# Optimization experiments

Measured on AMD Instinct MI355X. Metric: run time of the kernel, lower is better.

## Reference

```python
import jax, jax.numpy as jnp
import numpy as np

B, N, D, H, T, DFF, OUT = 32, 256, 512, 8, 60, 2048, 2
EPS = 1e-5


def _mha(q, k, v, Wq, Wk, Wv, Wo, bq, bk, bv, bo):
    # torch nn.MultiheadAttention (batch_first): x @ W.T + b projections
    Bq, Lq, Dm = q.shape
    dh = Dm // H
    scale = 1.0 / np.sqrt(dh).astype(np.float32)
    qh = (q @ Wq.T + bq).reshape(Bq, Lq, H, dh).transpose(0, 2, 1, 3)
    kh = (k @ Wk.T + bk).reshape(Bq, k.shape[1], H, dh).transpose(0, 2, 1, 3)
    vh = (v @ Wv.T + bv).reshape(Bq, v.shape[1], H, dh).transpose(0, 2, 1, 3)
    a = jax.nn.softmax(jnp.einsum('bhqd,bhkd->bhqk', qh, kh) * scale, axis=-1)
    o = jnp.einsum('bhqk,bhkd->bhqd', a, vh).transpose(0, 2, 1, 3).reshape(Bq, Lq, Dm)
    return o @ Wo.T + bo


def _ln(x, w, b):
    m = x.mean(-1, keepdims=True)
    v = ((x - m) ** 2).mean(-1, keepdims=True)
    return (x - m) / jnp.sqrt(v + EPS) * w + b


def setup_inputs() -> dict:
    key = jax.random.key(0)
    ks = iter(jax.random.split(key, 64))

    def rn(shape, s=0.05):
        return jax.random.normal(next(ks), shape, dtype=jnp.float32) * s

    inp = {
        'H_v_all': rn((B, N, D), 1.0),
        'H_v0_init': rn((B, 1, 1, D), 1.0),
        'pe': rn((1, T, D), 1.0),  # positional_encoding parameter
    }
    # s_* : spatial_attn;  sa_* : decoder self-attn;  ca_* : decoder cross-attn
    for p in ('s', 'sa', 'ca'):
        for m in ('Wq', 'Wk', 'Wv', 'Wo'):
            inp[f'{p}_{m}'] = rn((D, D))
        for m in ('bq', 'bk', 'bv', 'bo'):
            inp[f'{p}_{m}'] = jnp.zeros((D,), jnp.float32)
    for i in (1, 2, 3):
        inp[f'ln{i}_w'] = jnp.ones((D,), jnp.float32)
        inp[f'ln{i}_b'] = jnp.zeros((D,), jnp.float32)
    inp['W1'] = rn((DFF, D)); inp['b1'] = jnp.zeros((DFF,), jnp.float32)
    inp['W2'] = rn((D, DFF)); inp['b2'] = jnp.zeros((D,), jnp.float32)
    inp['Wout'] = rn((OUT, D)); inp['bout'] = jnp.zeros((OUT,), jnp.float32)
    return inp


def reference(H_v_all, H_v0_init, pe,
              s_Wq, s_Wk, s_Wv, s_Wo, s_bq, s_bk, s_bv, s_bo,
              sa_Wq, sa_Wk, sa_Wv, sa_Wo, sa_bq, sa_bk, sa_bv, sa_bo,
              ca_Wq, ca_Wk, ca_Wv, ca_Wo, ca_bq, ca_bk, ca_bv, ca_bo,
              ln1_w, ln1_b, ln2_w, ln2_b, ln3_w, ln3_b,
              W1, b1, W2, b2, Wout, bout):

    def dec_layer(x, mem):
        # post-norm TransformerDecoderLayer, no masks (non-causal), relu FFN, eval (no dropout)
        sa = _mha(x, x, x, sa_Wq, sa_Wk, sa_Wv, sa_Wo, sa_bq, sa_bk, sa_bv, sa_bo)
        x = _ln(x + sa, ln1_w, ln1_b)
        ca = _mha(x, mem, mem, ca_Wq, ca_Wk, ca_Wv, ca_Wo, ca_bq, ca_bk, ca_bv, ca_bo)
        x = _ln(x + ca, ln2_w, ln2_b)
        ff = jax.nn.relu(x @ W1.T + b1) @ W2.T + b2
        return _ln(x + ff, ln3_w, ln3_b)

    tgt = H_v0_init  # (B, 1, 1, D), grows along dim 2
    outputs = []
    for t in range(T):
        tgt_pe = tgt + pe[:, :t + 1][:, None]        # (B,1,t+1,D)
        tgt_step = tgt_pe.reshape(B, t + 1, D)
        ctx = _mha(tgt_step[:, -1:, :], H_v_all, H_v_all,
                   s_Wq, s_Wk, s_Wv, s_Wo, s_bq, s_bk, s_bv, s_bo)
        decoded = dec_layer(tgt_step, H_v_all)
        nxt = decoded[:, -1:, :] + ctx               # (B,1,D)
        tgt = jnp.concatenate([tgt, nxt[:, None]], axis=2)
        outputs.append(nxt[:, None])                 # (B,1,1,D)
    out_seq = jnp.concatenate(outputs, axis=2)       # (B,1,T,D)
    return out_seq @ Wout.T + bout                   # (B,1,T,2)
```

## Files before the change

kernel.cpp:

```cpp
#include <hip/hip_runtime.h>


#define NB 32
#define NN 256
#define DD 512
#define NH 8
#define DH 64
#define TT 60
#define DF 2048
#define NBLK 256
#define NTHR 512

typedef unsigned short ushort_t;
typedef _Float16 half2v __attribute__((ext_vector_type(2)));

constexpr size_t SZ_KV  = (size_t)NB * NN * DD;
constexpr size_t SZ_ROW = (size_t)NB * DD;
constexpr size_t SZ_PAR = (size_t)NB * NH * DD;
constexpr size_t OFF_KS32 = 0;
constexpr size_t OFF_VS32 = SZ_KV;
constexpr size_t OFF_KC32 = 2 * SZ_KV;
constexpr size_t OFF_VC32 = 3 * SZ_KV;
constexpr size_t OFF_X    = 0;
constexpr size_t OFF_U1P  = OFF_X   + SZ_ROW;
constexpr size_t OFF_U2P  = OFF_U1P + SZ_PAR;
constexpr size_t OFF_U3P  = OFF_U2P + SZ_PAR;
constexpr size_t OFF_CTP0 = OFF_U3P + SZ_PAR;
constexpr size_t OFF_CTP1 = OFF_CTP0 + SZ_PAR;
constexpr size_t OFF_BF   = 4 * SZ_KV;
constexpr size_t UOFF_KST = 0;
constexpr size_t UOFF_KCT = SZ_KV;
constexpr size_t UOFF_VSH = 2 * SZ_KV;
constexpr size_t UOFF_VCH = 3 * SZ_KV;
constexpr size_t UOFF_W8  = 4 * SZ_KV;
constexpr size_t UOFF_W1  = UOFF_W8 + 8ull * DD * DD;
constexpr size_t UOFF_W2  = UOFF_W1 + (size_t)DD * DF;
constexpr size_t UEND     = UOFF_W2 + (size_t)DF * DD;
constexpr size_t OFF_FLG  = OFF_BF + (UEND + 1) / 2;

constexpr unsigned DYN_LDS = 131072;

__device__ __forceinline__ float ldg_a(const float* p) {
  return __hip_atomic_load(p, __ATOMIC_RELAXED, __HIP_MEMORY_SCOPE_AGENT);
}
__device__ __forceinline__ void stg_a(float* p, float v) {
  __hip_atomic_store(p, v, __ATOMIC_RELAXED, __HIP_MEMORY_SCOPE_AGENT);
}
__device__ __forceinline__ unsigned f2pk(float a, float b) {
  return __builtin_bit_cast(unsigned, __builtin_amdgcn_cvt_pkrtz(a, b));
}
__device__ __forceinline__ ushort_t f2h(float a) {
  return (ushort_t)(f2pk(a, 0.f) & 0xffffu);
}
__device__ __forceinline__ float h2f(ushort_t u) {
  return (float)__builtin_bit_cast(_Float16, u);
}
__device__ __forceinline__ float fdot2u(unsigned a, unsigned b, float c) {
  return __builtin_amdgcn_fdot2(__builtin_bit_cast(half2v, a),
                                __builtin_bit_cast(half2v, b), c, false);
}

struct Params {
  const float *pe;
  const float *sa_bq, *sa_bk, *sa_bv, *s_bq, *sa_bo, *s_bo, *ca_bq, *ca_bo;
  const float *ln1w, *ln1b, *ln2w, *ln2b, *ln3w, *ln3b;
  const float *b1, *b2, *Wout, *bout;
  const ushort_t *w8, *w1b, *w2b;
  const ushort_t *KsT, *KcT, *VsH, *VcH;
  float *xcur, *u1p, *u2p, *u3p, *ctp0, *ctp1;
  float *out;
  unsigned *flags;
};

__device__ __forceinline__ void set_flag(unsigned* fl, int tid, int h,
                                         unsigned val) {
  __builtin_amdgcn_s_waitcnt(0);
  __syncthreads();
  if (tid == 0)
    __hip_atomic_store(&fl[h], val, __ATOMIC_RELAXED,
                       __HIP_MEMORY_SCOPE_AGENT);
}
__device__ __forceinline__ void wait_ge(unsigned* fl, int tid,
                                        unsigned target) {
  if (tid < 64) {
    bool wait = true;
    while (wait) {
      unsigned v = target;
      if (tid < 8)
        v = __hip_atomic_load(&fl[tid], __ATOMIC_RELAXED,
                              __HIP_MEMORY_SCOPE_AGENT);
      wait = __any(v < target);
    }
  }
  __syncthreads();
}

__global__ __launch_bounds__(512) void decode_persistent(Params P) {
  __shared__ __align__(16) float sX[2048];
  __shared__ __align__(16) float sPart[512];
  __shared__ float sAux[64];
  __shared__ __align__(16) unsigned xh[256];
  __shared__ __align__(16) unsigned ph[384];
  __shared__ __align__(16) ushort_t cacheK[TT * 78];
  __shared__ __align__(16) ushort_t cacheV[TT * 64];
  extern __shared__ __align__(16) unsigned dynLds[];
  unsigned* Ks_l = dynLds;
  unsigned* Kc_l = dynLds + 8192;
  ushort_t* Vs_l = (ushort_t*)(dynLds + 16384);
  ushort_t* Vc_l = Vs_l + 16384;

  int tid = threadIdx.x;
  int bid = blockIdx.x;
  int b = bid >> 3, h = bid & 7;
  int idx8 = bid;
  unsigned* fl = P.flags + b * 64;
  unsigned rnd = 0;

  {
    const uint4* gks = (const uint4*)((const unsigned*)P.KsT +
                       (((size_t)b * DD + h * DH) >> 1) * NN);
    const uint4* gkc = (const uint4*)((const unsigned*)P.KcT +
                       (((size_t)b * DD + h * DH) >> 1) * NN);
    const uint4* gvs = (const uint4*)(P.VsH + (size_t)idx8 * NN * DH);
    const uint4* gvc = (const uint4*)(P.VcH + (size_t)idx8 * NN * DH);
    uint4* dks = (uint4*)Ks_l;
    uint4* dkc = (uint4*)Kc_l;
    uint4* dvs = (uint4*)Vs_l;
    uint4* dvc = (uint4*)Vc_l;
    #pragma unroll
    for (int i = 0; i < 4; i++) {
      int idx = i * NTHR + tid;
      dks[idx] = gks[idx];
      dkc[idx] = gkc[idx];
      dvs[idx] = gvs[idx];
      dvc[idx] = gvc[idx];
    }
  }

  float x_f = ldg_a(P.xcur + (size_t)b * DD + tid);
  {
    float px = __shfl_xor(x_f, 1);
    if (!(tid & 1)) xh[tid >> 1] = f2pk(x_f, px);
  }
  __syncthreads();

  for (int t = 0; t < TT; t++) {
    {
      {
        int w = tid >> 6, c = tid & 63, m = w >> 1, half = w & 1;
        int col = h * DH + c;
        const uint2* wp = (const uint2*)(P.w8 + (size_t)m * DD * DD) + col;
        float acc = 0.f;
        #pragma unroll 8
        for (int kq = half * 64; kq < half * 64 + 64; kq++) {
          uint2 wv = wp[(size_t)kq * DD];
          uint2 xv = *(const uint2*)&xh[kq * 2];
          acc = fdot2u(wv.x, xv.x, acc);
          acc = fdot2u(wv.y, xv.y, acc);
        }
        sPart[tid] = acc;
      }
      __syncthreads();
      if (tid < 256) {
        int m = tid >> 6, c = tid & 63, col = h * DH + c;
        const float* bias = (m == 0) ? P.sa_bq : (m == 1) ? P.sa_bk
                          : (m == 2) ? P.sa_bv : P.s_bq;
        float val = sPart[(2 * m) * 64 + c] + sPart[(2 * m + 1) * 64 + c]
                    + bias[col];
        sX[512 + tid] = val;
        if (m == 1) cacheK[t * 78 + c] = f2h(val);
        if (m == 2) cacheV[t * 64 + c] = f2h(val);
      }
      __syncthreads();

      int L = t + 1;
      float* sQ  = sX + 512;
      float* sQs = sX + 704;
      float* sPb = sX + 768;
      if (tid < 64) {
        float e = 0.f;
        if (tid < L) {
          const unsigned* kl = (const unsigned*)(cacheK + (size_t)tid * 78);
          float a = 0.f;
          #pragma unroll 8
          for (int i = 0; i < 32; i++) {
            unsigned w = kl[i];
            a += sQ[2 * i] * h2f((ushort_t)(w & 0xffffu)) +
                 sQ[2 * i + 1] * h2f((ushort_t)(w >> 16));
          }
          e = __expf(a * 0.125f);
        }
        float s2 = e;
        #pragma unroll
        for (int s = 32; s >= 1; s >>= 1) s2 += __shfl_xor(s2, s);
        sPb[tid] = e * (1.f / s2);
        float o = 0.f;
        for (int j = 0; j < L; j++)
          o += sPb[j] * h2f(cacheV[j * 64 + tid]);
        float po = __shfl_xor(o, 1);
        if (!(tid & 1)) ph[32 + (tid >> 1)] = f2pk(o, po);
      } else if (tid < 320) {
        int n = tid - 64;
        float a = 0.f;
        #pragma unroll 8
        for (int i = 0; i < 32; i++) {
          unsigned w = Ks_l[i * NN + n];
          a += sQs[2 * i] * h2f((ushort_t)(w & 0xffffu)) +
               sQs[2 * i + 1] * h2f((ushort_t)(w >> 16));
        }
        sPart[n] = a * 0.125f;
      }
      __syncthreads();
      {
        float* u1p = P.u1p + ((size_t)b * NH + h) * DD;
        const uint2* wpa = (const uint2*)(P.w8 + 4ull * DD * DD) + tid;
        float acc1 = (h == 0) ? P.sa_bo[tid] + x_f : 0.f;
        #pragma unroll 8
        for (int j = 0; j < 16; j++) {
          int k4 = h * 16 + j;
          uint2 wv = wpa[(size_t)k4 * DD];
          uint2 x1 = *(const uint2*)&ph[32 + 2 * j];
          acc1 = fdot2u(wv.x, x1.x, acc1);
          acc1 = fdot2u(wv.y, x1.y, acc1);
        }
        stg_a(&u1p[tid], acc1);
      }
      set_flag(fl, tid, h, 3 * t + 1);
      float* sPr = sX + 1536;
      if (tid < 256) {
        float e = __expf(sPart[tid]);
        sPr[tid] = e;
        int w = tid >> 6;
        float s2 = e;
        #pragma unroll
        for (int s = 32; s >= 1; s >>= 1) s2 += __shfl_xor(s2, s);
        if ((tid & 63) == 0) sAux[4 + w] = s2;
      }
      __syncthreads();
      float* sB = sX + 1024;
      {
        int g = tid >> 6, d = tid & 63;
        float inv = 1.f / (sAux[4] + sAux[5] + sAux[6] + sAux[7]);
        const ushort_t* vp = Vs_l + (g * 32) * DH + d;
        float acc = 0.f;
        #pragma unroll 4
        for (int n = 0; n < 32; n++) acc += sPr[g * 32 + n] * h2f(vp[n * DH]);
        sB[tid] = acc * inv;
      }
      __syncthreads();
      if (tid < 64) {
        float o = 0.f;
        #pragma unroll
        for (int i = 0; i < 8; i++) o += sB[i * 64 + tid];
        float po = __shfl_xor(o, 1);
        if (!(tid & 1)) ph[64 + (tid >> 1)] = f2pk(o, po);
      }
      __syncthreads();
      {
        float* ctp = ((t & 1) ? P.ctp1 : P.ctp0) + ((size_t)b * NH + h) * DD;
        const uint2* wpb = (const uint2*)(P.w8 + 5ull * DD * DD) + tid;
        float acc2 = (h == 0) ? P.s_bo[tid] : 0.f;
        #pragma unroll 8
        for (int j = 0; j < 16; j++) {
          int k4 = h * 16 + j;
          uint2 wv2 = wpb[(size_t)k4 * DD];
          uint2 x2 = *(const uint2*)&ph[64 + 2 * j];
          acc2 = fdot2u(wv2.x, x2.x, acc2);
          acc2 = fdot2u(wv2.y, x2.y, acc2);
        }
        stg_a(&ctp[tid], acc2);
      }
    }

    float y1f;
    {
      wait_ge(fl, tid, 3 * t + 1);
      float u = 0.f;
      {
        const float* pp = P.u1p + (size_t)b * NH * DD + tid;
        #pragma unroll
        for (int i = 0; i < 8; i++) u += ldg_a(pp + i * DD);
      }
      {
        int w = tid >> 6;
        float s = u, q2 = u * u;
        #pragma unroll
        for (int m = 32; m >= 1; m >>= 1) { s += __shfl_xor(s, m); q2 += __shfl_xor(q2, m); }
        if ((tid & 63) == 0) { sAux[w] = s; sAux[8 + w] = q2; }
      }
      __syncthreads();
      {
        float ss = 0.f, qq = 0.f;
        #pragma unroll
        for (int i = 0; i < 8; i++) { ss += sAux[i]; qq += sAux[8 + i]; }
        float mean = ss * (1.f / 512.f);
        float inv = rsqrtf(qq * (1.f / 512.f) - mean * mean + 1e-5f);
        y1f = (u - mean) * inv * P.ln1w[tid] + P.ln1b[tid];
        float py = __shfl_xor(y1f, 1);
        if (!(tid & 1)) ph[128 + (tid >> 1)] = f2pk(y1f, py);
      }
      __syncthreads();
      {
        int c = tid & 63, w = tid >> 6, col = h * DH + c;
        const uint2* wp = (const uint2*)(P.w8 + 6ull * DD * DD) + col;
        float acc = 0.f;
        #pragma unroll 8
        for (int kq = w * 16; kq < w * 16 + 16; kq++) {
          uint2 wv = wp[(size_t)kq * DD];
          uint2 xv = *(const uint2*)&ph[128 + 2 * kq];
          acc = fdot2u(wv.x, xv.x, acc);
          acc = fdot2u(wv.y, xv.y, acc);
        }
        sPart[tid] = acc;
      }
      __syncthreads();
      if (tid < 64) {
        float o = 0.f;
        #pragma unroll
        for (int i = 0; i < 8; i++) o += sPart[i * 64 + tid];
        o += P.ca_bq[h * DH + tid];
        float po = __shfl_xor(o, 1);
        if (!(tid & 1)) ph[tid >> 1] = f2pk(o, po);
      }
      __syncthreads();
      {
        int n = tid & 255, dh2 = tid >> 8;
        float a = 0.f;
        #pragma unroll 8
        for (int dw = dh2 * 16; dw < dh2 * 16 + 16; dw++)
          a = fdot2u(Kc_l[dw * NN + n], ph[dw], a);
        sPart[tid] = a;
      }
      __syncthreads();
      float* sPr = sX + 1536;
      if (tid < 256) {
        float e = __expf((sPart[tid] + sPart[256 + tid]) * 0.125f);
        sPr[tid] = e;
        int w = tid >> 6;
        float s2 = e;
        #pragma unroll
        for (int s = 32; s >= 1; s >>= 1) s2 += __shfl_xor(s2, s);
        if ((tid & 63) == 0) sAux[4 + w] = s2;
      }
      __syncthreads();
      float* sB = sX + 1024;
      {
        int g = tid >> 6, d = tid & 63;
        float inv = 1.f / (sAux[4] + sAux[5] + sAux[6] + sAux[7]);
        const ushort_t* vp = Vc_l + (g * 32) * DH + d;
        float acc = 0.f;
        #pragma unroll 4
        for (int n = 0; n < 32; n++) acc += sPr[g * 32 + n] * h2f(vp[n * DH]);
        sB[tid] = acc * inv;
      }
      __syncthreads();
      if (tid < 64) {
        float o = 0.f;
        #pragma unroll
        for (int i = 0; i < 8; i++) o += sB[i * 64 + tid];
        float po = __shfl_xor(o, 1);
        if (!(tid & 1)) ph[32 + (tid >> 1)] = f2pk(o, po);
      }
      __syncthreads();
      {
        const uint2* wp = (const uint2*)(P.w8 + 7ull * DD * DD) + tid;
        float acc = (h == 0) ? P.ca_bo[tid] + y1f : 0.f;
        #pragma unroll 8
        for (int j = 0; j < 16; j++) {
          int k4 = h * 16 + j;
          uint2 wv = wp[(size_t)k4 * DD];
          uint2 xv = *(const uint2*)&ph[32 + 2 * j];
          acc = fdot2u(wv.x, xv.x, acc);
          acc = fdot2u(wv.y, xv.y, acc);
        }
        stg_a(&P.u2p[((size_t)b * NH + h) * DD + tid], acc);
      }
    }
    set_flag(fl, tid, h, 3 * t + 2);

    float zf;
    {
      wait_ge(fl, tid, 3 * t + 2);
      float v = 0.f;
      {
        const float* pp = P.u2p + (size_t)b * NH * DD + tid;
        #pragma unroll
        for (int i = 0; i < 8; i++) v += ldg_a(pp + i * DD);
      }
      {
        int w = tid >> 6;
        float s = v, q2 = v * v;
        #pragma unroll
        for (int m = 32; m >= 1; m >>= 1) { s += __shfl_xor(s, m); q2 += __shfl_xor(q2, m); }
        if ((tid & 63) == 0) { sAux[w] = s; sAux[8 + w] = q2; }
      }
      __syncthreads();
      {
        float ss = 0.f, qq = 0.f;
        #pragma unroll
        for (int i = 0; i < 8; i++) { ss += sAux[i]; qq += sAux[8 + i]; }
        float mean = ss * (1.f / 512.f);
        float inv = rsqrtf(qq * (1.f / 512.f) - mean * mean + 1e-5f);
        zf = (v - mean) * inv * P.ln2w[tid] + P.ln2b[tid];
        float pz = __shfl_xor(zf, 1);
        if (!(tid & 1)) ph[128 + (tid >> 1)] = f2pk(zf, pz);
      }
      __syncthreads();
      {
        int c = tid & 255, half = tid >> 8, col = h * 256 + c;
        const uint2* wp = (const uint2*)P.w1b + col;
        float acc = 0.f;
        #pragma unroll 8
        for (int kq = half * 64; kq < half * 64 + 64; kq++) {
          uint2 wv = wp[(size_t)kq * DF];
          uint2 xv = *(const uint2*)&ph[128 + 2 * kq];
          acc = fdot2u(wv.x, xv.x, acc);
          acc = fdot2u(wv.y, xv.y, acc);
        }
        sPart[tid] = acc;
      }
      __syncthreads();
      if (tid < 256) {
        float hv = fmaxf(sPart[tid] + sPart[256 + tid] + P.b1[h * 256 + tid], 0.f);
        float pv = __shfl_xor(hv, 1);
        if (!(tid & 1)) ph[tid >> 1] = f2pk(hv, pv);
      }
      __syncthreads();
      {
        const uint2* wp = (const uint2*)P.w2b + tid;
        float acc = (h == 0) ? zf + P.b2[tid] : 0.f;
        #pragma unroll 8
        for (int j = 0; j < 64; j++) {
          int k4 = h * 64 + j;
          uint2 wv = wp[(size_t)k4 * DD];
          uint2 xv = *(const uint2*)&ph[2 * j];
          acc = fdot2u(wv.x, xv.x, acc);
          acc = fdot2u(wv.y, xv.y, acc);
        }
        stg_a(&P.u3p[((size_t)b * NH + h) * DD + tid], acc);
      }
    }
    set_flag(fl, tid, h, 3 * t + 3);

    {
      wait_ge(fl, tid, 3 * t + 3);
      float u = 0.f, ctxv = 0.f;
      {
        const float* pp = P.u3p + (size_t)b * NH * DD + tid;
        const float* cp = ((t & 1) ? P.ctp1 : P.ctp0) + (size_t)b * NH * DD + tid;
        #pragma unroll
        for (int i = 0; i < 8; i++) { u += ldg_a(pp + i * DD); ctxv += ldg_a(cp + i * DD); }
      }
      {
        int w = tid >> 6;
        float s = u, q2 = u * u;
        #pragma unroll
        for (int m = 32; m >= 1; m >>= 1) { s += __shfl_xor(s, m); q2 += __shfl_xor(q2, m); }
        if ((tid & 63) == 0) { sAux[w] = s; sAux[8 + w] = q2; }
      }
      __syncthreads();
      float ss = 0.f, qq = 0.f;
      #pragma unroll
      for (int i = 0; i < 8; i++) { ss += sAux[i]; qq += sAux[8 + i]; }
      float mean = ss * (1.f / 512.f);
      float inv = rsqrtf(qq * (1.f / 512.f) - mean * mean + 1e-5f);
      float nxt = (u - mean) * inv * P.ln3w[tid] + P.ln3b[tid] + ctxv;
      float p = (t < TT - 1) ? P.pe[(size_t)(t + 1) * DD + tid] : 0.f;
      x_f = nxt + p;
      {
        float px = __shfl_xor(x_f, 1);
        if (!(tid & 1)) xh[tid >> 1] = f2pk(x_f, px);
      }
      if (h == 0) sX[tid] = nxt;
      __syncthreads();
      if (h == 0) {
        {
          int c = tid >> 8, l = tid & 255;
          float a = sX[l] * P.Wout[(size_t)c * DD + l] +
                    sX[l + 256] * P.Wout[(size_t)c * DD + l + 256];
          #pragma unroll
          for (int m = 32; m >= 1; m >>= 1) a += __shfl_xor(a, m);
          if ((tid & 63) == 0) sAux[16 + (tid >> 6)] = a;
        }
        __syncthreads();
        if (tid == 0)
          P.out[((size_t)b * TT + t) * 2 + 0] =
              sAux[16] + sAux[17] + sAux[18] + sAux[19] + P.bout[0];
        if (tid == 256)
          P.out[((size_t)b * TT + t) * 2 + 1] =
              sAux[20] + sAux[21] + sAux[22] + sAux[23] + P.bout[1];
      }
      __syncthreads();
    }
  }
  (void)rnd;
}

__global__ __launch_bounds__(256) void gemm_kv(
    const float* __restrict__ A,
    const float* __restrict__ W0, const float* __restrict__ W1_,
    const float* __restrict__ W2_, const float* __restrict__ W3_,
    const float* __restrict__ b0, const float* __restrict__ b1_,
    const float* __restrict__ b2_, const float* __restrict__ b3_,
    float* __restrict__ O0, float* __restrict__ O1,
    float* __restrict__ O2, float* __restrict__ O3) {
  __shared__ __align__(16) float As[8][128];
  __shared__ __align__(16) float Bs[8][128];
  int tid = threadIdx.x;
  int bx = blockIdx.x, by = blockIdx.y;
  int mm = bx >> 2;
  int col0 = (bx & 3) * 128;
  const float* W = mm == 0 ? W0 : mm == 1 ? W1_ : mm == 2 ? W2_ : W3_;
  const float* bias = mm == 0 ? b0 : mm == 1 ? b1_ : mm == 2 ? b2_ : b3_;
  float* O = mm == 0 ? O0 : mm == 1 ? O1 : mm == 2 ? O2 : O3;
  int tx = tid & 15, ty = tid >> 4;
  int m0 = by * 128;
  int lr = tid >> 1, lk = (tid & 1) * 4;
  const float* Ap = A + (size_t)(m0 + lr) * DD + lk;
  const float* Wp = W + (size_t)(col0 + lr) * DD + lk;
  float c[8][8] = {};
  for (int k0 = 0; k0 < DD; k0 += 8) {
    float4 av = *(const float4*)(Ap + k0);
    float4 wv = *(const float4*)(Wp + k0);
    __syncthreads();
    As[lk + 0][lr] = av.x; As[lk + 1][lr] = av.y; As[lk + 2][lr] = av.z; As[lk + 3][lr] = av.w;
    Bs[lk + 0][lr] = wv.x; Bs[lk + 1][lr] = wv.y; Bs[lk + 2][lr] = wv.z; Bs[lk + 3][lr] = wv.w;
    __syncthreads();
    #pragma unroll
    for (int k = 0; k < 8; k++) {
      float a[8], bb[8];
      *(float4*)&a[0] = *(const float4*)&As[k][ty * 8];
      *(float4*)&a[4] = *(const float4*)&As[k][ty * 8 + 4];
      *(float4*)&bb[0] = *(const float4*)&Bs[k][tx * 8];
      *(float4*)&bb[4] = *(const float4*)&Bs[k][tx * 8 + 4];
      #pragma unroll
      for (int i = 0; i < 8; i++)
        #pragma unroll
        for (int j = 0; j < 8; j++) c[i][j] += a[i] * bb[j];
    }
  }
  const float* bp = bias + col0 + tx * 8;
  for (int i = 0; i < 8; i++) {
    int row = m0 + ty * 8 + i;
    float* op = O + (size_t)row * DD + col0 + tx * 8;
    #pragma unroll
    for (int jq = 0; jq < 8; jq += 4) {
      float4 v;
      v.x = c[i][jq + 0] + bp[jq + 0];
      v.y = c[i][jq + 1] + bp[jq + 1];
      v.z = c[i][jq + 2] + bp[jq + 2];
      v.w = c[i][jq + 3] + bp[jq + 3];
      *(float4*)(op + jq) = v;
    }
  }
}

__global__ __launch_bounds__(256) void pack_kT(const float* __restrict__ Ks32,
                                               const float* __restrict__ Kc32,
                                               ushort_t* __restrict__ KsT,
                                               ushort_t* __restrict__ KcT) {
  int z = blockIdx.z;
  int b = z >> 1;
  const float* in = ((z & 1) ? Kc32 : Ks32) + (size_t)b * NN * DD;
  ushort_t* out = ((z & 1) ? KcT : KsT) + (size_t)b * NN * DD;
  int r0 = blockIdx.x * 32, c0 = blockIdx.y * 32;
  __shared__ float tile[32][33];
  int tid = threadIdx.x;
  int i = tid >> 3, j4 = (tid & 7) * 4;
  float4 v = *(const float4*)(in + (size_t)(r0 + i) * DD + c0 + j4);
  tile[i][j4] = v.x; tile[i][j4 + 1] = v.y; tile[i][j4 + 2] = v.z; tile[i][j4 + 3] = v.w;
  __syncthreads();
  int d = c0 + i;
  ushort_t* op = out + (size_t)(d >> 1) * (2 * NN) + 2 * (r0 + j4) + (d & 1);
  op[0] = f2h(tile[j4][i]);     op[2] = f2h(tile[j4 + 1][i]);
  op[4] = f2h(tile[j4 + 2][i]); op[6] = f2h(tile[j4 + 3][i]);
}

__global__ __launch_bounds__(256) void pack_vh(const float* __restrict__ Vs32,
                                               const float* __restrict__ Vc32,
                                               ushort_t* __restrict__ VsH,
                                               ushort_t* __restrict__ VcH) {
  const float* src = blockIdx.y ? Vc32 : Vs32;
  ushort_t* dst = blockIdx.y ? VcH : VsH;
  size_t idx = (size_t)blockIdx.x * 1024 + threadIdx.x * 4;
  float4 v = *(const float4*)(src + idx);
  int d512 = (int)(idx & 511);
  int n = (int)((idx >> 9) & 255);
  int b = (int)(idx >> 17);
  int h = d512 >> 6, d = d512 & 63;
  ushort_t* op = dst + (((size_t)(b * 8 + h) * NN + n) * DH + d);
  op[0] = f2h(v.x); op[1] = f2h(v.y); op[2] = f2h(v.z); op[3] = f2h(v.w);
}

struct PWItem { const float* in; ushort_t* out; int C; int K; };
struct PWArgs { PWItem m[10]; };
__global__ __launch_bounds__(256) void pack_w(PWArgs a) {
  PWItem it = a.m[blockIdx.y];
  int total = it.C * (it.K >> 2);
  int e = blockIdx.x * 256 + threadIdx.x;
  if (e >= total) return;
  int kd = it.K >> 2;
  int k4 = e % kd, col = e / kd;
  float4 v = *(const float4*)(it.in + (size_t)col * it.K + k4 * 4);
  unsigned lo = f2pk(v.x, v.y), hi = f2pk(v.z, v.w);
  ushort4 o;
  o.x = (ushort_t)(lo & 0xffffu); o.y = (ushort_t)(lo >> 16);
  o.z = (ushort_t)(hi & 0xffffu); o.w = (ushort_t)(hi >> 16);
  *((ushort4*)it.out + (size_t)k4 * it.C + col) = o;
}

__global__ __launch_bounds__(256) void init_x(const float* __restrict__ hv0,
                                              const float* __restrict__ pe,
                                              float* __restrict__ ws,
                                              unsigned* __restrict__ flags) {
  int i = blockIdx.x * 256 + threadIdx.x;
  ws[OFF_X + i] = hv0[i] + pe[i & (DD - 1)];
  if (i < 2048) flags[i] = 0u;
}

extern "C" void kernel_launch(void* const* d_in, const int* in_sizes, int n_in,
                              void* d_out, int out_size, void* d_ws, size_t ws_size,
                              hipStream_t stream) {
  const float* H_v_all = (const float*)d_in[0];
  const float* H_v0    = (const float*)d_in[1];
  const float* pe      = (const float*)d_in[2];
  const float* s_Wq = (const float*)d_in[3];
  const float* s_Wk = (const float*)d_in[4];
  const float* s_Wv = (const float*)d_in[5];
  const float* s_Wo = (const float*)d_in[6];
  const float* s_bq = (const float*)d_in[7];
  const float* s_bk = (const float*)d_in[8];
  const float* s_bv = (const float*)d_in[9];
  const float* s_bo = (const float*)d_in[10];
  const float* sa_Wq = (const float*)d_in[11];
  const float* sa_Wk = (const float*)d_in[12];
  const float* sa_Wv = (const float*)d_in[13];
  const float* sa_Wo = (const float*)d_in[14];
  const float* sa_bq = (const float*)d_in[15];
  const float* sa_bk = (const float*)d_in[16];
  const float* sa_bv = (const float*)d_in[17];
  const float* sa_bo = (const float*)d_in[18];
  const float* ca_Wq = (const float*)d_in[19];
  const float* ca_Wk = (const float*)d_in[20];
  const float* ca_Wv = (const float*)d_in[21];
  const float* ca_Wo = (const float*)d_in[22];
  const float* ca_bq = (const float*)d_in[23];
  const float* ca_bk = (const float*)d_in[24];
  const float* ca_bv = (const float*)d_in[25];
  const float* ca_bo = (const float*)d_in[26];
  const float* ln1w = (const float*)d_in[27];
  const float* ln1b = (const float*)d_in[28];
  const float* ln2w = (const float*)d_in[29];
  const float* ln2b = (const float*)d_in[30];
  const float* ln3w = (const float*)d_in[31];
  const float* ln3b = (const float*)d_in[32];
  const float* W1   = (const float*)d_in[33];
  const float* b1   = (const float*)d_in[34];
  const float* W2   = (const float*)d_in[35];
  const float* b2   = (const float*)d_in[36];
  const float* Wout = (const float*)d_in[37];
  const float* bout = (const float*)d_in[38];

  float* ws = (float*)d_ws;
  float* Ks32 = ws + OFF_KS32;
  float* Vs32 = ws + OFF_VS32;
  float* Kc32 = ws + OFF_KC32;
  float* Vc32 = ws + OFF_VC32;
  ushort_t* ub = (ushort_t*)(ws + OFF_BF);
  unsigned* flags = (unsigned*)(ws + OFF_FLG);

  hipLaunchKernelGGL(gemm_kv, dim3(16, 64), dim3(256), 0, stream,
                     H_v_all, s_Wk, s_Wv, ca_Wk, ca_Wv,
                     s_bk, s_bv, ca_bk, ca_bv, Ks32, Vs32, Kc32, Vc32);

  hipLaunchKernelGGL(pack_kT, dim3(8, 16, 64), dim3(256), 0, stream,
                     Ks32, Kc32, ub + UOFF_KST, ub + UOFF_KCT);
  hipLaunchKernelGGL(pack_vh, dim3((unsigned)(SZ_KV / 1024), 2), dim3(256), 0,
                     stream, Vs32, Vc32, ub + UOFF_VSH, ub + UOFF_VCH);

  PWArgs pw;
  pw.m[0] = {sa_Wq, ub + UOFF_W8 + 0ull * DD * DD, DD, DD};
  pw.m[1] = {sa_Wk, ub + UOFF_W8 + 1ull * DD * DD, DD, DD};
  pw.m[2] = {sa_Wv, ub + UOFF_W8 + 2ull * DD * DD, DD, DD};
  pw.m[3] = {s_Wq,  ub + UOFF_W8 + 3ull * DD * DD, DD, DD};
  pw.m[4] = {sa_Wo, ub + UOFF_W8 + 4ull * DD * DD, DD, DD};
  pw.m[5] = {s_Wo,  ub + UOFF_W8 + 5ull * DD * DD, DD, DD};
  pw.m[6] = {ca_Wq, ub + UOFF_W8 + 6ull * DD * DD, DD, DD};
  pw.m[7] = {ca_Wo, ub + UOFF_W8 + 7ull * DD * DD, DD, DD};
  pw.m[8] = {W1, ub + UOFF_W1, DF, DD};
  pw.m[9] = {W2, ub + UOFF_W2, DD, DF};
  hipLaunchKernelGGL(pack_w, dim3(1024, 10), dim3(256), 0, stream, pw);

  hipLaunchKernelGGL(init_x, dim3(64), dim3(256), 0, stream,
                     H_v0, pe, ws, flags);

  static bool attr_set = false;
  if (!attr_set) {
    hipFuncSetAttribute((const void*)decode_persistent,
                        hipFuncAttributeMaxDynamicSharedMemorySize, DYN_LDS);
    attr_set = true;
  }

  Params P;
  P.pe = pe;
  P.sa_bq = sa_bq; P.sa_bk = sa_bk; P.sa_bv = sa_bv; P.s_bq = s_bq;
  P.sa_bo = sa_bo; P.s_bo = s_bo; P.ca_bq = ca_bq; P.ca_bo = ca_bo;
  P.ln1w = ln1w; P.ln1b = ln1b; P.ln2w = ln2w; P.ln2b = ln2b;
  P.ln3w = ln3w; P.ln3b = ln3b;
  P.b1 = b1; P.b2 = b2; P.Wout = Wout; P.bout = bout;
  P.w8 = ub + UOFF_W8; P.w1b = ub + UOFF_W1; P.w2b = ub + UOFF_W2;
  P.KsT = ub + UOFF_KST; P.KcT = ub + UOFF_KCT;
  P.VsH = ub + UOFF_VSH; P.VcH = ub + UOFF_VCH;
  P.xcur = ws + OFF_X;
  P.u1p = ws + OFF_U1P; P.u2p = ws + OFF_U2P; P.u3p = ws + OFF_U3P;
  P.ctp0 = ws + OFF_CTP0; P.ctp1 = ws + OFF_CTP1;
  P.out = (float*)d_out;
  P.flags = flags;

  void* kargs[] = { (void*)&P };
  hipLaunchCooperativeKernel((void*)decode_persistent, dim3(NBLK), dim3(NTHR),
                             kargs, DYN_LDS, stream);
}
```

Before: 2.082 ms.

## Use packed fp16 dot products in KV GEMM and tune decode unrolling

The K/V projection GEMM now packs A and W into fp16 pairs in shared memory and accumulates with fdot2 instead of fp32 FMAs. This halves LDS traffic and FMA count in that kernel, at the cost of lower precision in the keys and values. The persistent decode kernel gets a launch-bounds occupancy hint and fully unrolled or wider-unrolled matvec loops to raise memory-level parallelism. The occupancy hint risks register spills.

After: 4.397 ms. 2.11x slower.

```diff
diff --git a/kernel.cpp b/kernel.cpp
--- a/kernel.cpp
+++ b/kernel.cpp
@@ -95,7 +95,7 @@
   __syncthreads();
 }
 
-__global__ __launch_bounds__(512) void decode_persistent(Params P) {
+__global__ __launch_bounds__(512, 2) void decode_persistent(Params P) {
   __shared__ __align__(16) float sX[2048];
   __shared__ __align__(16) float sPart[512];
   __shared__ float sAux[64];
@@ -114,7 +114,6 @@
   int b = bid >> 3, h = bid & 7;
   int idx8 = bid;
   unsigned* fl = P.flags + b * 64;
-  unsigned rnd = 0;
 
   {
     const uint4* gks = (const uint4*)((const unsigned*)P.KsT +
@@ -151,7 +150,7 @@
         int col = h * DH + c;
         const uint2* wp = (const uint2*)(P.w8 + (size_t)m * DD * DD) + col;
         float acc = 0.f;
-        #pragma unroll 8
+        #pragma unroll 16
         for (int kq = half * 64; kq < half * 64 + 64; kq++) {
           uint2 wv = wp[(size_t)kq * DD];
           uint2 xv = *(const uint2*)&xh[kq * 2];
@@ -215,7 +214,7 @@
         float* u1p = P.u1p + ((size_t)b * NH + h) * DD;
         const uint2* wpa = (const uint2*)(P.w8 + 4ull * DD * DD) + tid;
         float acc1 = (h == 0) ? P.sa_bo[tid] + x_f : 0.f;
-        #pragma unroll 8
+        #pragma unroll
         for (int j = 0; j < 16; j++) {
           int k4 = h * 16 + j;
           uint2 wv = wpa[(size_t)k4 * DD];
@@ -260,7 +259,7 @@
         float* ctp = ((t & 1) ? P.ctp1 : P.ctp0) + ((size_t)b * NH + h) * DD;
         const uint2* wpb = (const uint2*)(P.w8 + 5ull * DD * DD) + tid;
         float acc2 = (h == 0) ? P.s_bo[tid] : 0.f;
-        #pragma unroll 8
+        #pragma unroll
         for (int j = 0; j < 16; j++) {
           int k4 = h * 16 + j;
           uint2 wv2 = wpb[(size_t)k4 * DD];
@@ -304,8 +303,9 @@
         int c = tid & 63, w = tid >> 6, col = h * DH + c;
         const uint2* wp = (const uint2*)(P.w8 + 6ull * DD * DD) + col;
         float acc = 0.f;
-        #pragma unroll 8
-        for (int kq = w * 16; kq < w * 16 + 16; kq++) {
+        #pragma unroll
+        for (int j = 0; j < 16; j++) {
+          int kq = w * 16 + j;
           uint2 wv = wp[(size_t)kq * DD];
           uint2 xv = *(const uint2*)&ph[128 + 2 * kq];
           acc = fdot2u(wv.x, xv.x, acc);
@@ -365,7 +365,7 @@
       {
         const uint2* wp = (const uint2*)(P.w8 + 7ull * DD * DD) + tid;
         float acc = (h == 0) ? P.ca_bo[tid] + y1f : 0.f;
-        #pragma unroll 8
+        #pragma unroll
         for (int j = 0; j < 16; j++) {
           int k4 = h * 16 + j;
           uint2 wv = wp[(size_t)k4 * DD];
@@ -410,7 +410,7 @@
         int c = tid & 255, half = tid >> 8, col = h * 256 + c;
         const uint2* wp = (const uint2*)P.w1b + col;
         float acc = 0.f;
-        #pragma unroll 8
+        #pragma unroll 16
         for (int kq = half * 64; kq < half * 64 + 64; kq++) {
           uint2 wv = wp[(size_t)kq * DF];
           uint2 xv = *(const uint2*)&ph[128 + 2 * kq];
@@ -429,7 +429,7 @@
       {
         const uint2* wp = (const uint2*)P.w2b + tid;
         float acc = (h == 0) ? zf + P.b2[tid] : 0.f;
-        #pragma unroll 8
+        #pragma unroll 16
         for (int j = 0; j < 64; j++) {
           int k4 = h * 64 + j;
           uint2 wv = wp[(size_t)k4 * DD];
@@ -493,7 +493,6 @@
       __syncthreads();
     }
   }
-  (void)rnd;
 }
 
 __global__ __launch_bounds__(256) void gemm_kv(
@@ -504,8 +503,8 @@
     const float* __restrict__ b2_, const float* __restrict__ b3_,
     float* __restrict__ O0, float* __restrict__ O1,
     float* __restrict__ O2, float* __restrict__ O3) {
-  __shared__ __align__(16) float As[8][128];
-  __shared__ __align__(16) float Bs[8][128];
+  __shared__ __align__(16) unsigned As2[4][128];
+  __shared__ __align__(16) unsigned Bs2[4][128];
   int tid = threadIdx.x;
   int bx = blockIdx.x, by = blockIdx.y;
   int mm = bx >> 2;
@@ -523,20 +522,24 @@
     float4 av = *(const float4*)(Ap + k0);
     float4 wv = *(const float4*)(Wp + k0);
     __syncthreads();
-    As[lk + 0][lr] = av.x; As[lk + 1][lr] = av.y; As[lk + 2][lr] = av.z; As[lk + 3][lr] = av.w;
-    Bs[lk + 0][lr] = wv.x; Bs[lk + 1][lr] = wv.y; Bs[lk + 2][lr] = wv.z; Bs[lk + 3][lr] = wv.w;
+    int kk = lk >> 1;
+    As2[kk + 0][lr] = f2pk(av.x, av.y);
+    As2[kk + 1][lr] = f2pk(av.z, av.w);
+    Bs2[kk + 0][lr] = f2pk(wv.x, wv.y);
+    Bs2[kk + 1][lr] = f2pk(wv.z, wv.w);
     __syncthreads();
     #pragma unroll
-    for (int k = 0; k < 8; k++) {
-      float a[8], bb[8];
-      *(float4*)&a[0] = *(const float4*)&As[k][ty * 8];
-      *(float4*)&a[4] = *(const float4*)&As[k][ty * 8 + 4];
-      *(float4*)&bb[0] = *(const float4*)&Bs[k][tx * 8];
-      *(float4*)&bb[4] = *(const float4*)&Bs[k][tx * 8 + 4];
+    for (int k2 = 0; k2 < 4; k2++) {
+      unsigned a2[8], b2[8];
+      *(uint4*)&a2[0] = *(const uint4*)&As2[k2][ty * 8];
+      *(uint4*)&a2[4] = *(const uint4*)&As2[k2][ty * 8 + 4];
+      *(uint4*)&b2[0] = *(const uint4*)&Bs2[k2][tx * 8];
+      *(uint4*)&b2[4] = *(const uint4*)&Bs2[k2][tx * 8 + 4];
       #pragma unroll
       for (int i = 0; i < 8; i++)
         #pragma unroll
-        for (int j = 0; j < 8; j++) c[i][j] += a[i] * bb[j];
+        for (int j = 0; j < 8; j++)
+          c[i][j] = fdot2u(a2[i], b2[j], c[i][j]);
     }
   }
   const float* bp = bias + col0 + tx * 8;
```
